# Kernel tuning notes

Measured on AMD Instinct MI355X. Metric: run time of the kernel, lower is better.

The kernel has to match this reference:

```python
import jax, jax.numpy as jnp
import numpy as np

TAU = 2.0      # membrane time constant
V_TH = 1.0     # spike threshold (v_reset = 0, hard reset)
T_STEPS = 4    # num_steps

@jax.custom_vjp
def heaviside_atan(x):
    # forward: Heaviside; backward: spikingjelly ATan surrogate (alpha=2)
    return (x >= 0.0).astype(x.dtype)

def _h_fwd(x):
    return heaviside_atan(x), x

def _h_bwd(x, g):
    alpha = 2.0
    return (g * (alpha / 2.0) / (1.0 + (jnp.pi / 2.0 * alpha * x) ** 2),)

heaviside_atan.defvjp(_h_fwd, _h_bwd)

def lif_multistep(x_seq):
    # spikingjelly LIFNode, step_mode='m', decay_input=True, v_reset=0, detach_reset=True
    def step(v, x):
        v = v + (x - v) / TAU                      # charge
        s = heaviside_atan(v - V_TH)               # fire (surrogate grad)
        v = v * (1.0 - jax.lax.stop_gradient(s))   # hard reset, detached spike
        return v, s
    v0 = jnp.zeros_like(x_seq[0])
    _, spikes = jax.lax.scan(step, v0, x_seq)
    return spikes

def setup_inputs() -> dict:
    key = jax.random.key(0)
    k0, k1, k2 = jax.random.split(key, 3)
    B, L, C, D, NL = 16, 512, 128, 1024, 2
    inputs = jax.random.normal(k0, (B, L, C), jnp.float32)
    enc_W = jax.random.normal(k1, (C, D), jnp.float32) / np.sqrt(C).astype(np.float32)
    enc_b = jnp.zeros((D,), jnp.float32)
    W_cells = jax.random.normal(k2, (NL, D, D), jnp.float32) / np.sqrt(D).astype(np.float32)
    b_cells = jnp.zeros((NL, D), jnp.float32)
    return {"inputs": inputs, "enc_W": enc_W, "enc_b": enc_b,
            "W_cells": W_cells, "b_cells": b_cells}

def reference(inputs, enc_W, enc_b, W_cells, b_cells):
    # temporal spike encoder: repeat input over T steps, LIF-encode to spikes
    x = jnp.swapaxes(inputs, 1, 2)                       # [B, C, L]
    x = jnp.broadcast_to(x[None], (T_STEPS,) + x.shape)  # [T, B, C, L]
    h = lif_multistep(x)
    h = jnp.swapaxes(h, -2, -1)                          # [T, B, L, C]
    # encoder linear + init LIF
    h = lif_multistep(h @ enc_W + enc_b)                 # [T, B, L, D]
    # stacked SpikeRNNCells: Linear(D,D) -> multistep LIF
    for i in range(W_cells.shape[0]):
        h = lif_multistep(h @ W_cells[i] + b_cells[i])
    out = h.mean(0)                                      # [B, L, D]
    return out, out.mean(axis=1)                         # ([B,L,D], [B,D])
```

## Files before the change

### kernel.cpp

```cpp
#include <hip/hip_runtime.h>
#include <hip/hip_bf16.h>
#include <stdint.h>

#define TSTEPS 4

typedef __bf16 bf16_t;
typedef __attribute__((ext_vector_type(8))) __bf16 bf16x8;
typedef __attribute__((ext_vector_type(16))) float f32x16;
typedef __attribute__((ext_vector_type(4))) unsigned short ushort4v;

union frag_u { bf16x8 v; uint32_t d[4]; unsigned short u[8]; };

#define WT_VM5_LG0  0x075
#define WT_VM4      0xF74
#define WT_VM0_LG0  0x070


__global__ void spike_encode_i8(const float* __restrict__ x,
                                uint4* __restrict__ s1)
{
    const int C = 128;
    int tid = blockIdx.x * blockDim.x + threadIdx.x;
    int row = tid & 31;
    int kb  = (tid >> 5) & 7;
    int m_blk = tid >> 8;
    int m = m_blk * 32 + row;
    const float* px = x + (size_t)m * C + kb * 16;
    float xv[16];
#pragma unroll
    for (int j = 0; j < 16; j += 4) {
        float4 t4 = *(const float4*)(px + j);
        xv[j] = t4.x; xv[j+1] = t4.y; xv[j+2] = t4.z; xv[j+3] = t4.w;
    }
    float v[16];
#pragma unroll
    for (int j = 0; j < 16; ++j) v[j] = 0.0f;
#pragma unroll
    for (int t = 0; t < TSTEPS; ++t) {
        uint32_t dw[4] = {0u, 0u, 0u, 0u};
#pragma unroll
        for (int j = 0; j < 16; ++j) {
            float vv = __fadd_rn(v[j], __fmul_rn(__fsub_rn(xv[j], v[j]), 0.5f));
            bool sp = (vv >= 1.0f);
            dw[j >> 2] |= sp ? (0x3Fu << ((j & 3) * 8)) : 0u;
            v[j] = sp ? 0.0f : vv;
        }
        uint4 o; o.x = dw[0]; o.y = dw[1]; o.z = dw[2]; o.w = dw[3];
        s1[((size_t)(m_blk * 8 + kb) * 4 + t) * 32 + row] = o;
    }
}

__global__ void split_transpose_all(const float* __restrict__ enc_W,
                                    const float* __restrict__ W_cells,
                                    bf16_t* __restrict__ W1h, bf16_t* __restrict__ W1l,
                                    bf16_t* __restrict__ W2h, bf16_t* __restrict__ W2l,
                                    bf16_t* __restrict__ W3h, bf16_t* __restrict__ W3l)
{
    const int N = 1024;
    const float* W;
    bf16_t *hi, *lo;
    int K;
    if (blockIdx.z == 0) {
        if (blockIdx.x >= 4) return;
        W = enc_W; hi = W1h; lo = W1l; K = 128;
    } else if (blockIdx.z == 1) {
        W = W_cells; hi = W2h; lo = W2l; K = 1024;
    } else {
        W = W_cells + (size_t)1024 * 1024; hi = W3h; lo = W3l; K = 1024;
    }
    const int NKB = K >> 4;
    __shared__ float tile[32][33];
    int k0 = blockIdx.x * 32, n0 = blockIdx.y * 32;
    int tx = threadIdx.x & 31, ty = threadIdx.x >> 5;
    for (int kk = ty; kk < 32; kk += 8)
        tile[kk][tx] = W[(size_t)(k0 + kk) * N + n0 + tx];
    __syncthreads();

    const int nn = tx;
    const int oc = ty;
    const int o2 = oc & 3;
    const bool isLo = (oc >> 2) != 0;
    const int kblk = (k0 >> 4) + (o2 >> 1);
    const int lane_in_packet = nn + 32 * (o2 & 1);

    frag_u f;
#pragma unroll
    for (int j = 0; j < 8; ++j) {
        float wv = tile[o2 * 8 + j][nn];
        bf16_t h = (bf16_t)wv;
        bf16_t l = (bf16_t)(wv - (float)h);
        f.v[j] = isLo ? (bf16_t)(2.0f * (float)l)
                      : (bf16_t)(2.0f * (float)h);
    }
    bf16_t* dst = (isLo ? lo : hi)
        + ((size_t)((n0 + nn) >> 5) * NKB + kblk) * 512 + lane_in_packet * 8;
    *(bf16x8*)dst = f.v;
}

template <int K, bool LAST>
__global__ __launch_bounds__(256, 4)
void gemm_lif_mfma(const uint8_t* __restrict__ Abytes,
                   const bf16_t* __restrict__ Bh,
                   const bf16_t* __restrict__ Bl,
                   const float* __restrict__ bias,
                   uint8_t* __restrict__ Sbytes,
                   float* __restrict__ Out,
                   int M, int N)
{
    constexpr int NKB = K >> 4;
    __shared__ __align__(16) uint8_t ldsB[2][4096];
    __shared__ __align__(8) unsigned short sh[4][256];

    const int tid = threadIdx.x;
    const int lane = tid & 63;
    const int wid = tid >> 6;
    const int l31 = lane & 31;
    const int half = lane >> 5;

    const int bid = blockIdx.x;
    const int xcd = bid & 7;
    const int j   = bid >> 3;
    const int nh   = j >> 7;
    const int r    = j & 127;
    const int mloc = r >> 3;
    const int n_t  = nh * 8 + (r & 7);
    const int m_t  = xcd * 16 + mloc;

    const int m0 = m_t * 64, n0 = n_t * 64;
    const int wave_m = (wid & 1) * 32;
    const int wave_n = (wid >> 1) * 32;
    const int m_blk = (m0 + wave_m) >> 5;
    const int n_blk = (n0 + wave_n) >> 5;

    const uint8_t* pA = Abytes + (size_t)m_blk * NKB * 4 * 512 + l31 * 16 + half * 8;

    const uint8_t* stage_src = (const uint8_t*)(((wid & 1) ? Bl : Bh)
        + (size_t)((n0 >> 5) + (wid >> 1)) * NKB * 512) + (lane << 4);
    const uint8_t* ldsRd = &ldsB[0][0] + ((wid >> 1) << 11) + (lane << 4);

    f32x16 acc[TSTEPS];
#pragma unroll
    for (int t = 0; t < TSTEPS; ++t)
        for (int rr = 0; rr < 16; ++rr) acc[t][rr] = 0.0f;

    uint2 fm[2][4];

#define STAGE(kb_, b_)                                                        \
    __builtin_amdgcn_global_load_lds(                                         \
        (const __attribute__((address_space(1))) uint32_t*)                   \
            (stage_src + (size_t)(kb_) * 1024),                               \
        (__attribute__((address_space(3))) uint32_t*)(&ldsB[b_][wid << 10]),  \
        16, 0, 0);

#define LOADA(kb_, s_) {                                                     \
        fm[s_][0] = *(const uint2*)(pA + ((size_t)(kb_) * 4 + 0) * 512);     \
        fm[s_][1] = *(const uint2*)(pA + ((size_t)(kb_) * 4 + 1) * 512);     \
        fm[s_][2] = *(const uint2*)(pA + ((size_t)(kb_) * 4 + 2) * 512);     \
        fm[s_][3] = *(const uint2*)(pA + ((size_t)(kb_) * 4 + 3) * 512);     \
    }

#define EXPANDF(a_, f_) {                                                    \
        (f_).d[0] = __builtin_amdgcn_perm((a_).x, 0u, 0x05000400u);          \
        (f_).d[1] = __builtin_amdgcn_perm((a_).x, 0u, 0x07000600u);          \
        (f_).d[2] = __builtin_amdgcn_perm((a_).y, 0u, 0x05000400u);          \
        (f_).d[3] = __builtin_amdgcn_perm((a_).y, 0u, 0x07000600u);          \
    }

#define MFMAS(s_, fhv_, flv_) {                                              \
        frag_u af0, af1, af2, af3;                                           \
        EXPANDF(fm[s_][0], af0);                                             \
        EXPANDF(fm[s_][1], af1);                                             \
        EXPANDF(fm[s_][2], af2);                                             \
        EXPANDF(fm[s_][3], af3);                                             \
        acc[0] = __builtin_amdgcn_mfma_f32_32x32x16_bf16(af0.v, fhv_, acc[0], 0, 0, 0); \
        acc[1] = __builtin_amdgcn_mfma_f32_32x32x16_bf16(af1.v, fhv_, acc[1], 0, 0, 0); \
        acc[2] = __builtin_amdgcn_mfma_f32_32x32x16_bf16(af2.v, fhv_, acc[2], 0, 0, 0); \
        acc[3] = __builtin_amdgcn_mfma_f32_32x32x16_bf16(af3.v, fhv_, acc[3], 0, 0, 0); \
        acc[0] = __builtin_amdgcn_mfma_f32_32x32x16_bf16(af0.v, flv_, acc[0], 0, 0, 0); \
        acc[1] = __builtin_amdgcn_mfma_f32_32x32x16_bf16(af1.v, flv_, acc[1], 0, 0, 0); \
        acc[2] = __builtin_amdgcn_mfma_f32_32x32x16_bf16(af2.v, flv_, acc[2], 0, 0, 0); \
        acc[3] = __builtin_amdgcn_mfma_f32_32x32x16_bf16(af3.v, flv_, acc[3], 0, 0, 0); \
    }

#define STEP(kb_, p_) {                                                      \
        STAGE((kb_) + 1, (p_) ^ 1);                                          \
        LOADA((kb_) + 1, (p_) ^ 1);                                          \
        bf16x8 fhv = *(const bf16x8*)(ldsRd + (p_) * 4096);                  \
        bf16x8 flv = *(const bf16x8*)(ldsRd + (p_) * 4096 + 1024);           \
        __builtin_amdgcn_s_waitcnt(WT_VM5_LG0);                              \
        asm volatile("" ::: "memory");                                       \
        MFMAS(p_, fhv, flv);                                                 \
        __builtin_amdgcn_s_waitcnt(WT_VM4);                                  \
        asm volatile("" ::: "memory");                                       \
        __builtin_amdgcn_s_barrier();                                        \
        asm volatile("" ::: "memory");                                       \
    }

    STAGE(0, 0);
    LOADA(0, 0);
    __builtin_amdgcn_s_waitcnt(WT_VM4);
    asm volatile("" ::: "memory");
    __builtin_amdgcn_s_barrier();
    asm volatile("" ::: "memory");

    for (int kb = 0; kb < NKB - 2; kb += 2) {
        STEP(kb + 0, 0);
        STEP(kb + 1, 1);
    }
    STEP(NKB - 2, 0);
    {
        bf16x8 fhv = *(const bf16x8*)(ldsRd + 4096);
        bf16x8 flv = *(const bf16x8*)(ldsRd + 4096 + 1024);
        __builtin_amdgcn_s_waitcnt(WT_VM0_LG0);
        asm volatile("" ::: "memory");
        MFMAS(1, fhv, flv);
    }

#undef STEP
#undef MFMAS
#undef EXPANDF
#undef LOADA
#undef STAGE

    const float bv = bias[n0 + wave_n + l31];
    f32x16 vmem;
#pragma unroll
    for (int rr = 0; rr < 16; ++rr) vmem[rr] = 0.0f;
    uint64_t bits = 0ull;
    unsigned short* myt = &sh[wid][0];

    const int NKBo = N >> 4;
    const int kbase = (n0 + wave_n) >> 4;

    for (int t = 0; t < TSTEPS; ++t) {
#pragma unroll
        for (int rr = 0; rr < 16; ++rr) {
            float y = __fadd_rn(acc[t][rr], bv);
            float vv = vmem[rr];
            vv = __fadd_rn(vv, __fmul_rn(__fsub_rn(y, vv), 0.5f));
            bool sp = (vv >= 1.0f);
            vmem[rr] = sp ? 0.0f : vv;
            if (LAST) {
                bits |= sp ? (1ull << (rr * 4 + t)) : 0ull;
            } else {
                unsigned long long b = __ballot(sp);
                if (l31 == 0) {
                    uint32_t hb = (uint32_t)(b >> (half * 32));
                    int rowi = (rr & 3) + 8 * (rr >> 2) + 4 * half;
                    myt[(rowi * 2 + 0) * 4 + t] = (unsigned short)hb;
                    myt[(rowi * 2 + 1) * 4 + t] = (unsigned short)(hb >> 16);
                }
            }
        }
    }

    if (LAST) {
#pragma unroll
        for (int rr = 0; rr < 16; ++rr) {
            int m_r = (rr & 3) + 8 * (rr >> 2) + 4 * half;
            int m = m0 + wave_m + m_r;
            int n = n0 + wave_n + l31;
            int cnt = __popc((unsigned)((bits >> (rr * 4)) & 0xFull));
            Out[(size_t)m * N + n] = 0.25f * (float)cnt;
        }
    } else {
        const ushort4v pk = *(const ushort4v*)&myt[(l31 * 2 + half) * 4];
#pragma unroll
        for (int t = 0; t < TSTEPS; ++t) {
            uint32_t m16 = pk[t];
            uint4 o;
            o.x = (((m16      ) & 0xFu) * 0x00204081u & 0x01010101u) * 0x3Fu;
            o.y = (((m16 >>  4) & 0xFu) * 0x00204081u & 0x01010101u) * 0x3Fu;
            o.z = (((m16 >>  8) & 0xFu) * 0x00204081u & 0x01010101u) * 0x3Fu;
            o.w = (((m16 >> 12) & 0xFu) * 0x00204081u & 0x01010101u) * 0x3Fu;
            *(uint4*)(Sbytes + ((((size_t)m_blk * NKBo + kbase + half) * 4 + t)
                                * 32 + l31) * 16) = o;
        }
    }
}

__global__ void zero_out2(float* __restrict__ out2, int n)
{
    int i = blockIdx.x * blockDim.x + threadIdx.x;
    if (i < n) out2[i] = 0.0f;
}

__global__ void mean_over_L_atomic(const float* __restrict__ out,
                                   float* __restrict__ out2,
                                   int B, int L, int D)
{
    int id = blockIdx.x * blockDim.x + threadIdx.x;
    int bd = id & (B * D - 1);
    int chunk = id >> 14;
    int b = bd >> 10, d = bd & (D - 1);
    const float* p = out + (size_t)b * L * D + (size_t)chunk * 64 * D + d;
    float s = 0.0f;
#pragma unroll 8
    for (int l = 0; l < 64; ++l) s += p[(size_t)l * D];
    atomicAdd(out2 + bd, s * (1.0f / 512.0f));
}

extern "C" void kernel_launch(void* const* d_in, const int* in_sizes, int n_in,
                              void* d_out, int out_size, void* d_ws, size_t ws_size,
                              hipStream_t stream)
{
    const float* inputs  = (const float*)d_in[0];
    const float* enc_W   = (const float*)d_in[1];
    const float* enc_b   = (const float*)d_in[2];
    const float* W_cells = (const float*)d_in[3];
    const float* b_cells = (const float*)d_in[4];

    const int B = 16, L = 512, C = 128, D = 1024;
    const int M = B * L;

    char* ws = (char*)d_ws;
    size_t off = 0;
    uint8_t* s1 = (uint8_t*)(ws + off);
    off += (size_t)(M / 32) * (C / 16) * 4 * 32 * 16;
    bf16_t* W1h = (bf16_t*)(ws + off); off += (size_t)C * D * 2;
    bf16_t* W1l = (bf16_t*)(ws + off); off += (size_t)C * D * 2;
    bf16_t* W2h = (bf16_t*)(ws + off); off += (size_t)D * D * 2;
    bf16_t* W2l = (bf16_t*)(ws + off); off += (size_t)D * D * 2;
    bf16_t* W3h = (bf16_t*)(ws + off); off += (size_t)D * D * 2;
    bf16_t* W3l = (bf16_t*)(ws + off); off += (size_t)D * D * 2;
    uint8_t* h0 = (uint8_t*)(ws + off);
    off += (size_t)(M / 32) * (D / 16) * 4 * 32 * 16;
    uint8_t* h1 = (uint8_t*)(ws + off);

    float* out  = (float*)d_out;
    float* out2 = out + (size_t)M * D;

    split_transpose_all<<<dim3(32, 32, 3), 256, 0, stream>>>(
        enc_W, W_cells, W1h, W1l, W2h, W2l, W3h, W3l);

    spike_encode_i8<<<256, 256, 0, stream>>>(inputs, (uint4*)s1);

    zero_out2<<<(B * D + 255) / 256, 256, 0, stream>>>(out2, B * D);

    const int nblocks = (M / 64) * (D / 64);
    gemm_lif_mfma<128, false><<<nblocks, 256, 0, stream>>>(
        s1, W1h, W1l, enc_b, h0, nullptr, M, D);
    gemm_lif_mfma<1024, false><<<nblocks, 256, 0, stream>>>(
        h0, W2h, W2l, b_cells, h1, nullptr, M, D);
    gemm_lif_mfma<1024, true><<<nblocks, 256, 0, stream>>>(
        h1, W3h, W3l, b_cells + D, nullptr, out, M, D);

    mean_over_L_atomic<<<(B * D * 8) / 256, 256, 0, stream>>>(
        out, out2, B, L, D);
}
```

Measured before the change: 317.1 us.

## Enlarge GEMM-LIF block tile to 128x128 with 16 waves and two k-blocks per barrier

Each workgroup now covers a 128x128 output tile with 16 waves (1024 threads) instead of 64x64 with 4 waves. Each pipeline phase stages two k-blocks of the hi/lo B weights into LDS, so the kernel hits a barrier half as often. The aim is more reuse of B in LDS across more M rows, fewer barriers, and less global traffic for the B tile. The costs are a larger LDS footprint, register pressure from doubled A prefetch, and a grid of only 512 blocks with 16 waves each, which may hurt occupancy and load balance.

```diff
diff --git a/kernel.cpp b/kernel.cpp
--- a/kernel.cpp
+++ b/kernel.cpp
@@ -11,9 +11,10 @@
 
 union frag_u { bf16x8 v; uint32_t d[4]; unsigned short u[8]; };
 
-#define WT_VM5_LG0  0x075
-#define WT_VM4      0xF74
-#define WT_VM0_LG0  0x070
+#define WT_VM9_LG0 0x079
+#define WT_VM8     0xF78
+#define WT_LG0     0xC07F
+#define WT_VM0_LG0 0x070
 
 
 __global__ void spike_encode_i8(const float* __restrict__ x,
@@ -98,7 +99,7 @@
 }
 
 template <int K, bool LAST>
-__global__ __launch_bounds__(256, 4)
+__global__ __launch_bounds__(1024, 4)
 void gemm_lif_mfma(const uint8_t* __restrict__ Abytes,
                    const bf16_t* __restrict__ Bh,
                    const bf16_t* __restrict__ Bl,
@@ -108,8 +109,9 @@
                    int M, int N)
 {
     constexpr int NKB = K >> 4;
-    __shared__ __align__(16) uint8_t ldsB[2][4096];
-    __shared__ __align__(8) unsigned short sh[4][256];
+    constexpr int NP  = NKB >> 1;
+    __shared__ __align__(16) uint8_t ldsB[2][2][8192];
+    __shared__ __align__(8) unsigned short sh[16][256];
 
     const int tid = threadIdx.x;
     const int lane = tid & 63;
@@ -120,43 +122,51 @@
     const int bid = blockIdx.x;
     const int xcd = bid & 7;
     const int j   = bid >> 3;
-    const int nh   = j >> 7;
-    const int r    = j & 127;
-    const int mloc = r >> 3;
-    const int n_t  = nh * 8 + (r & 7);
-    const int m_t  = xcd * 16 + mloc;
-
-    const int m0 = m_t * 64, n0 = n_t * 64;
-    const int wave_m = (wid & 1) * 32;
-    const int wave_n = (wid >> 1) * 32;
+    const int nh   = j >> 5;
+    const int r    = j & 31;
+    const int mloc = r >> 2;
+    const int n_t  = nh * 4 + (r & 3);
+    const int m_t  = xcd * 8 + mloc;
+
+    const int m0 = m_t * 128, n0 = n_t * 128;
+    const int wave_m = (wid & 3) * 32;
+    const int wave_n = (wid >> 2) * 32;
     const int m_blk = (m0 + wave_m) >> 5;
-    const int n_blk = (n0 + wave_n) >> 5;
 
     const uint8_t* pA = Abytes + (size_t)m_blk * NKB * 4 * 512 + l31 * 16 + half * 8;
 
-    const uint8_t* stage_src = (const uint8_t*)(((wid & 1) ? Bl : Bh)
-        + (size_t)((n0 >> 5) + (wid >> 1)) * NKB * 512) + (lane << 4);
-    const uint8_t* ldsRd = &ldsB[0][0] + ((wid >> 1) << 11) + (lane << 4);
+    const int kbip = wid >> 3;
+    const int cch  = wid & 7;
+    const uint8_t* stage_src = (const uint8_t*)(((cch & 1) ? Bl : Bh)
+        + (size_t)((n0 >> 5) + (cch >> 1)) * NKB * 512)
+        + (size_t)kbip * 1024 + (lane << 4);
+    uint8_t* stage_dst = &ldsB[0][0][0] + kbip * 8192 + cch * 1024;
+    const uint8_t* ldsRd = &ldsB[0][0][0] + ((wid >> 2) << 11) + (lane << 4);
 
     f32x16 acc[TSTEPS];
 #pragma unroll
     for (int t = 0; t < TSTEPS; ++t)
         for (int rr = 0; rr < 16; ++rr) acc[t][rr] = 0.0f;
 
-    uint2 fm[2][4];
-
-#define STAGE(kb_, b_)                                                        \
+    uint2 fm[2][2][4];
+
+#define STAGE(pair_, b_)                                                      \
     __builtin_amdgcn_global_load_lds(                                         \
         (const __attribute__((address_space(1))) uint32_t*)                   \
-            (stage_src + (size_t)(kb_) * 1024),                               \
-        (__attribute__((address_space(3))) uint32_t*)(&ldsB[b_][wid << 10]),  \
+            (stage_src + (size_t)(pair_) * 2048),                             \
+        (__attribute__((address_space(3))) uint32_t*)                         \
+            (stage_dst + (b_) * 16384),                                       \
         16, 0, 0);
 
-#define LOADA(kb_, s_) {                                                     \
-        fm[s_][0] = *(const uint2*)(pA + ((size_t)(kb_) * 4 + 0) * 512);     \
-        fm[s_][1] = *(const uint2*)(pA + ((size_t)(kb_) * 4 + 1) * 512);     \
-        fm[s_][2] = *(const uint2*)(pA + ((size_t)(kb_) * 4 + 2) * 512);     \
-        fm[s_][3] = *(const uint2*)(pA + ((size_t)(kb_) * 4 + 3) * 512);     \
+#define LOADA2(pair_, s_) {                                                  \
+        fm[s_][0][0] = *(const uint2*)(pA + ((size_t)(pair_)*8 + 0) * 512);  \
+        fm[s_][0][1] = *(const uint2*)(pA + ((size_t)(pair_)*8 + 1) * 512);  \
+        fm[s_][0][2] = *(const uint2*)(pA + ((size_t)(pair_)*8 + 2) * 512);  \
+        fm[s_][0][3] = *(const uint2*)(pA + ((size_t)(pair_)*8 + 3) * 512);  \
+        fm[s_][1][0] = *(const uint2*)(pA + ((size_t)(pair_)*8 + 4) * 512);  \
+        fm[s_][1][1] = *(const uint2*)(pA + ((size_t)(pair_)*8 + 5) * 512);  \
+        fm[s_][1][2] = *(const uint2*)(pA + ((size_t)(pair_)*8 + 6) * 512);  \
+        fm[s_][1][3] = *(const uint2*)(pA + ((size_t)(pair_)*8 + 7) * 512);  \
     }
 
 #define EXPANDF(a_, f_) {                                                    \
@@ -166,12 +176,12 @@
         (f_).d[3] = __builtin_amdgcn_perm((a_).y, 0u, 0x07000600u);          \
     }
 
-#define MFMAS(s_, fhv_, flv_) {                                              \
+#define MFMAS(s_, kbip_, fhv_, flv_) {                                       \
         frag_u af0, af1, af2, af3;                                           \
-        EXPANDF(fm[s_][0], af0);                                             \
-        EXPANDF(fm[s_][1], af1);                                             \
-        EXPANDF(fm[s_][2], af2);                                             \
-        EXPANDF(fm[s_][3], af3);                                             \
+        EXPANDF(fm[s_][kbip_][0], af0);                                      \
+        EXPANDF(fm[s_][kbip_][1], af1);                                      \
+        EXPANDF(fm[s_][kbip_][2], af2);                                      \
+        EXPANDF(fm[s_][kbip_][3], af3);                                      \
         acc[0] = __builtin_amdgcn_mfma_f32_32x32x16_bf16(af0.v, fhv_, acc[0], 0, 0, 0); \
         acc[1] = __builtin_amdgcn_mfma_f32_32x32x16_bf16(af1.v, fhv_, acc[1], 0, 0, 0); \
         acc[2] = __builtin_amdgcn_mfma_f32_32x32x16_bf16(af2.v, fhv_, acc[2], 0, 0, 0); \
@@ -182,44 +192,54 @@
         acc[3] = __builtin_amdgcn_mfma_f32_32x32x16_bf16(af3.v, flv_, acc[3], 0, 0, 0); \
     }
 
-#define STEP(kb_, p_) {                                                      \
-        STAGE((kb_) + 1, (p_) ^ 1);                                          \
-        LOADA((kb_) + 1, (p_) ^ 1);                                          \
-        bf16x8 fhv = *(const bf16x8*)(ldsRd + (p_) * 4096);                  \
-        bf16x8 flv = *(const bf16x8*)(ldsRd + (p_) * 4096 + 1024);           \
-        __builtin_amdgcn_s_waitcnt(WT_VM5_LG0);                              \
+#define PHASE(pair_, b_) {                                                   \
+        STAGE((pair_) + 1, (b_) ^ 1);                                        \
+        LOADA2((pair_) + 1, (b_) ^ 1);                                       \
+        bf16x8 fh0 = *(const bf16x8*)(ldsRd + (b_) * 16384);                 \
+        bf16x8 fl0 = *(const bf16x8*)(ldsRd + (b_) * 16384 + 1024);          \
+        __builtin_amdgcn_s_waitcnt(WT_VM9_LG0);                              \
         asm volatile("" ::: "memory");                                       \
-        MFMAS(p_, fhv, flv);                                                 \
-        __builtin_amdgcn_s_waitcnt(WT_VM4);                                  \
+        MFMAS(b_, 0, fh0, fl0);                                              \
+        bf16x8 fh1 = *(const bf16x8*)(ldsRd + (b_) * 16384 + 8192);          \
+        bf16x8 fl1 = *(const bf16x8*)(ldsRd + (b_) * 16384 + 8192 + 1024);   \
+        __builtin_amdgcn_s_waitcnt(WT_LG0);                                  \
+        asm volatile("" ::: "memory");                                       \
+        MFMAS(b_, 1, fh1, fl1);                                              \
+        __builtin_amdgcn_s_waitcnt(WT_VM8);                                  \
         asm volatile("" ::: "memory");                                       \
         __builtin_amdgcn_s_barrier();                                        \
         asm volatile("" ::: "memory");                                       \
     }
 
     STAGE(0, 0);
-    LOADA(0, 0);
-    __builtin_amdgcn_s_waitcnt(WT_VM4);
+    LOADA2(0, 0);
+    __builtin_amdgcn_s_waitcnt(WT_VM8);
     asm volatile("" ::: "memory");
     __builtin_amdgcn_s_barrier();
     asm volatile("" ::: "memory");
 
-    for (int kb = 0; kb < NKB - 2; kb += 2) {
-        STEP(kb + 0, 0);
-        STEP(kb + 1, 1);
-    }
-    STEP(NKB - 2, 0);
+    for (int p = 0; p < NP - 2; p += 2) {
+        PHASE(p + 0, 0);
+        PHASE(p + 1, 1);
+    }
+    PHASE(NP - 2, 0);
     {
-        bf16x8 fhv = *(const bf16x8*)(ldsRd + 4096);
-        bf16x8 flv = *(const bf16x8*)(ldsRd + 4096 + 1024);
+        bf16x8 fh0 = *(const bf16x8*)(ldsRd + 16384);
+        bf16x8 fl0 = *(const bf16x8*)(ldsRd + 16384 + 1024);
         __builtin_amdgcn_s_waitcnt(WT_VM0_LG0);
         asm volatile("" ::: "memory");
-        MFMAS(1, fhv, flv);
-    }
-
-#undef STEP
+        MFMAS(1, 0, fh0, fl0);
+        bf16x8 fh1 = *(const bf16x8*)(ldsRd + 16384 + 8192);
+        bf16x8 fl1 = *(const bf16x8*)(ldsRd + 16384 + 8192 + 1024);
+        __builtin_amdgcn_s_waitcnt(WT_LG0);
+        asm volatile("" ::: "memory");
+        MFMAS(1, 1, fh1, fl1);
+    }
+
+#undef PHASE
 #undef MFMAS
 #undef EXPANDF
-#undef LOADA
+#undef LOADA2
 #undef STAGE
 
     const float bv = bias[n0 + wave_n + l31];
@@ -337,12 +357,12 @@
 
     zero_out2<<<(B * D + 255) / 256, 256, 0, stream>>>(out2, B * D);
 
-    const int nblocks = (M / 64) * (D / 64);
-    gemm_lif_mfma<128, false><<<nblocks, 256, 0, stream>>>(
+    const int nblocks = (M / 128) * (D / 128);
+    gemm_lif_mfma<128, false><<<nblocks, 1024, 0, stream>>>(
         s1, W1h, W1l, enc_b, h0, nullptr, M, D);
-    gemm_lif_mfma<1024, false><<<nblocks, 256, 0, stream>>>(
+    gemm_lif_mfma<1024, false><<<nblocks, 1024, 0, stream>>>(
         h0, W2h, W2l, b_cells, h1, nullptr, M, D);
-    gemm_lif_mfma<1024, true><<<nblocks, 256, 0, stream>>>(
+    gemm_lif_mfma<1024, true><<<nblocks, 1024, 0, stream>>>(
         h1, W3h, W3l, b_cells + D, nullptr, out, M, D);
 
     mean_over_L_atomic<<<(B * D * 8) / 256, 256, 0, stream>>>(
```

After: 351.6 us. 10.9% more time.

## Fuse mean-over-L into last GEMM epilogue and prefetch B fragments earlier

Applied to the files above, without the earlier changes.

The separate mean_over_L kernel is removed. The last GEMM epilogue now sums its per-lane spike rates, combines the two half-waves with a shuffle, and atomically adds the partial mean into out2. This saves one launch and one full re-read of the output tensor, at the cost of more atomics from the GEMM. The main loop also issues the LDS loads of the B fragments for the next stage right after the barrier, so they overlap the next step's waits, and it raises wave priority around the MFMA block with s_setprio.

```diff
diff --git a/kernel.cpp b/kernel.cpp
--- a/kernel.cpp
+++ b/kernel.cpp
@@ -131,6 +131,7 @@
     const int wave_n = (wid >> 1) * 32;
     const int m_blk = (m0 + wave_m) >> 5;
     const int n_blk = (n0 + wave_n) >> 5;
+    (void)n_blk;
 
     const uint8_t* pA = Abytes + (size_t)m_blk * NKB * 4 * 512 + l31 * 16 + half * 8;
 
@@ -185,15 +186,17 @@
 #define STEP(kb_, p_) {                                                      \
         STAGE((kb_) + 1, (p_) ^ 1);                                          \
         LOADA((kb_) + 1, (p_) ^ 1);                                          \
-        bf16x8 fhv = *(const bf16x8*)(ldsRd + (p_) * 4096);                  \
-        bf16x8 flv = *(const bf16x8*)(ldsRd + (p_) * 4096 + 1024);           \
         __builtin_amdgcn_s_waitcnt(WT_VM5_LG0);                              \
         asm volatile("" ::: "memory");                                       \
-        MFMAS(p_, fhv, flv);                                                 \
+        __builtin_amdgcn_s_setprio(1);                                       \
+        MFMAS(p_, cfh, cfl);                                                 \
+        __builtin_amdgcn_s_setprio(0);                                       \
         __builtin_amdgcn_s_waitcnt(WT_VM4);                                  \
         asm volatile("" ::: "memory");                                       \
         __builtin_amdgcn_s_barrier();                                        \
         asm volatile("" ::: "memory");                                       \
+        cfh = *(const bf16x8*)(ldsRd + (((p_) ^ 1)) * 4096);                 \
+        cfl = *(const bf16x8*)(ldsRd + (((p_) ^ 1)) * 4096 + 1024);          \
     }
 
     STAGE(0, 0);
@@ -202,6 +205,8 @@
     asm volatile("" ::: "memory");
     __builtin_amdgcn_s_barrier();
     asm volatile("" ::: "memory");
+    bf16x8 cfh = *(const bf16x8*)(ldsRd);
+    bf16x8 cfl = *(const bf16x8*)(ldsRd + 1024);
 
     for (int kb = 0; kb < NKB - 2; kb += 2) {
         STEP(kb + 0, 0);
@@ -209,11 +214,11 @@
     }
     STEP(NKB - 2, 0);
     {
-        bf16x8 fhv = *(const bf16x8*)(ldsRd + 4096);
-        bf16x8 flv = *(const bf16x8*)(ldsRd + 4096 + 1024);
         __builtin_amdgcn_s_waitcnt(WT_VM0_LG0);
         asm volatile("" ::: "memory");
-        MFMAS(1, fhv, flv);
+        __builtin_amdgcn_s_setprio(1);
+        MFMAS(1, cfh, cfl);
+        __builtin_amdgcn_s_setprio(0);
     }
 
 #undef STEP
@@ -255,13 +260,23 @@
     }
 
     if (LAST) {
+        float psum = 0.0f;
 #pragma unroll
         for (int rr = 0; rr < 16; ++rr) {
             int m_r = (rr & 3) + 8 * (rr >> 2) + 4 * half;
             int m = m0 + wave_m + m_r;
             int n = n0 + wave_n + l31;
             int cnt = __popc((unsigned)((bits >> (rr * 4)) & 0xFull));
-            Out[(size_t)m * N + n] = 0.25f * (float)cnt;
+            float val = 0.25f * (float)cnt;
+            Out[(size_t)m * N + n] = val;
+            psum += val;
+        }
+        psum += __shfl_xor(psum, 32, 64);
+        if (half == 0) {
+            float* out2 = Out + (size_t)M * N;
+            int b = m0 >> 9;
+            int n = n0 + wave_n + l31;
+            atomicAdd(out2 + (size_t)b * N + n, psum * (1.0f / 512.0f));
         }
     } else {
         const ushort4v pk = *(const ushort4v*)&myt[(l31 * 2 + half) * 4];
@@ -283,21 +298,6 @@
 {
     int i = blockIdx.x * blockDim.x + threadIdx.x;
     if (i < n) out2[i] = 0.0f;
-}
-
-__global__ void mean_over_L_atomic(const float* __restrict__ out,
-                                   float* __restrict__ out2,
-                                   int B, int L, int D)
-{
-    int id = blockIdx.x * blockDim.x + threadIdx.x;
-    int bd = id & (B * D - 1);
-    int chunk = id >> 14;
-    int b = bd >> 10, d = bd & (D - 1);
-    const float* p = out + (size_t)b * L * D + (size_t)chunk * 64 * D + d;
-    float s = 0.0f;
-#pragma unroll 8
-    for (int l = 0; l < 64; ++l) s += p[(size_t)l * D];
-    atomicAdd(out2 + bd, s * (1.0f / 512.0f));
 }
 
 extern "C" void kernel_launch(void* const* d_in, const int* in_sizes, int n_in,
@@ -344,7 +344,4 @@
         h0, W2h, W2l, b_cells, h1, nullptr, M, D);
     gemm_lif_mfma<1024, true><<<nblocks, 256, 0, stream>>>(
         h1, W3h, W3l, b_cells + D, nullptr, out, M, D);
-
-    mean_over_L_atomic<<<(B * D * 8) / 256, 256, 0, stream>>>(
-        out, out2, B, L, D);
-}
+}
```

Result: no change. 315.6 us (-0.5%).
